# Optimization experiments

Measured on AMD Instinct MI355X. Metric: run time of the kernel, lower is better.

The kernel has to match this reference:

```python
import jax, jax.numpy as jnp
import numpy as np

C_IN, C_OUT, K, DG, PAD = 256, 256, 3, 2, 1
EPS = 1e-5


def setup_inputs() -> dict:
    key = jax.random.key(0)
    k = jax.random.split(key, 8)
    B, H, W = 4, 64, 64
    x = jax.random.normal(k[0], (B, C_IN, H, W), jnp.float32)
    # offset/mask conv (DCNv2 pack): 3 * dg * k * k output channels
    w_off = jax.random.normal(k[1], (3 * DG * K * K, C_IN, K, K), jnp.float32) * 0.01
    b_off = jnp.zeros((3 * DG * K * K,), jnp.float32)
    # main deformable conv weight
    w = jax.random.normal(k[2], (C_OUT, C_IN, K, K), jnp.float32) * (1.0 / np.sqrt(C_IN * K * K))
    b = jnp.zeros((C_OUT,), jnp.float32)
    # BatchNorm (eval mode: running stats)
    gamma = jnp.ones((C_OUT,), jnp.float32)
    beta = jnp.zeros((C_OUT,), jnp.float32)
    running_mean = jax.random.normal(k[3], (C_OUT,), jnp.float32) * 0.1
    running_var = jax.random.uniform(k[4], (C_OUT,), jnp.float32, 0.5, 1.5)
    return dict(x=x, w_off=w_off, b_off=b_off, w=w, b=b, gamma=gamma, beta=beta,
                running_mean=running_mean, running_var=running_var)


def _conv2d_same(x, w, b):
    y = jax.lax.conv_general_dilated(x, w, (1, 1), 'SAME',
                                     dimension_numbers=('NCHW', 'OIHW', 'NCHW'))
    return y + b[None, :, None, None]


def _deform_conv(x, w_off, b_off, w, b):
    B, C, H, W = x.shape
    K2 = K * K
    Cg = C // DG
    # offsets + modulation mask from internal conv (DCNv2 pack)
    om = _conv2d_same(x, w_off, b_off)            # [B, 3*DG*K2, H, W]
    o1, o2, m = jnp.split(om, 3, axis=1)
    mask = jax.nn.sigmoid(m).reshape(B, DG, 1, K2, H * W)
    off_y = o1.reshape(B, DG, K2, H, W)
    off_x = o2.reshape(B, DG, K2, H, W)
    # base sampling grid: output pixel + kernel tap - pad
    ki = jnp.arange(K)
    ky = (jnp.repeat(ki, K) - PAD).astype(jnp.float32)   # [K2]
    kx = (jnp.tile(ki, K) - PAD).astype(jnp.float32)     # [K2]
    py = off_y + ky[:, None, None] + jnp.arange(H, dtype=jnp.float32)[None, :, None]
    px = off_x + kx[:, None, None] + jnp.arange(W, dtype=jnp.float32)[None, None, :]
    y0 = jnp.floor(py)
    x0 = jnp.floor(px)
    ly = (py - y0).reshape(B, DG, 1, K2, H * W)
    lx = (px - x0).reshape(B, DG, 1, K2, H * W)
    y0i = y0.astype(jnp.int32)
    x0i = x0.astype(jnp.int32)
    xg = x.reshape(B, DG, Cg, H * W)

    def gather(yi, xi):
        # zero-padded bilinear corner gather, per deformable group
        valid = (yi >= 0) & (yi < H) & (xi >= 0) & (xi < W)
        lin = jnp.clip(yi, 0, H - 1) * W + jnp.clip(xi, 0, W - 1)
        v = jnp.take_along_axis(xg[:, :, :, None, :],
                                lin.reshape(B, DG, 1, K2, H * W), axis=-1)
        return v * valid.reshape(B, DG, 1, K2, H * W)

    val = (gather(y0i, x0i) * (1 - ly) * (1 - lx)
           + gather(y0i, x0i + 1) * (1 - ly) * lx
           + gather(y0i + 1, x0i) * ly * (1 - lx)
           + gather(y0i + 1, x0i + 1) * ly * lx)
    val = val * mask                               # [B, DG, Cg, K2, H*W]
    wr = w.reshape(C_OUT, DG, Cg, K2)
    out = jnp.einsum('bgckn,ogck->bon', val, wr).reshape(B, C_OUT, H, W)
    return out + b[None, :, None, None]


def reference(x, w_off, b_off, w, b, gamma, beta, running_mean, running_var):
    y = _deform_conv(x, w_off, b_off, w, b)
    inv = gamma / jnp.sqrt(running_var + EPS)
    y = (y - running_mean[None, :, None, None]) * inv[None, :, None, None] + beta[None, :, None, None]
    return jax.nn.relu(y)
```

## Files before the change

### kernel.cpp

```cpp
#include <hip/hip_runtime.h>
#include <math.h>

typedef __bf16 bf16x8 __attribute__((ext_vector_type(8)));
typedef float  f32x4  __attribute__((ext_vector_type(4)));
typedef int    i32x4  __attribute__((ext_vector_type(4)));

#define MFMA16(a, b, c) __builtin_amdgcn_mfma_f32_16x16x32_bf16((a), (b), (c), 0, 0, 0)

#define ATIDX(r, c) ((r) * 128 + (((c) ^ ((r) & 7)) * 8))

__global__ __launch_bounds__(256) void setup_kernel(
    const float* __restrict__ x, const float* __restrict__ w,
    const float* __restrict__ w_off, const float* __restrict__ bconv,
    const float* __restrict__ gamma, const float* __restrict__ beta,
    const float* __restrict__ mean, const float* __restrict__ var,
    __bf16* __restrict__ xT, __bf16* __restrict__ wFragD,
    __bf16* __restrict__ wFragO, float* __restrict__ sc,
    float* __restrict__ sh) {
  int t = threadIdx.x;
  if (blockIdx.x < 1024) {
    __shared__ float xs[64][65];
    int b = blockIdx.x >> 8, y = (blockIdx.x >> 2) & 63, cc = blockIdx.x & 3;
    const float* xb = x + (((size_t)b * 256 + cc * 64) * 64 + y) * 64;
    #pragma unroll
    for (int r = 0; r < 4; ++r) {
      int cl = r * 16 + (t >> 4), xc = (t & 15) * 4;
      f32x4 v = *(const f32x4*)(xb + (size_t)cl * 4096 + xc);
      xs[cl][xc] = v.x; xs[cl][xc + 1] = v.y;
      xs[cl][xc + 2] = v.z; xs[cl][xc + 3] = v.w;
    }
    __syncthreads();
    __bf16* dst = xT + (((size_t)b * 64 + y) * 64) * 256 + cc * 64;
    #pragma unroll
    for (int it = 0; it < 2; ++it) {
      int w2 = t + it * 256;
      int xc = w2 >> 3, cl8 = (w2 & 7) * 8;
      bf16x8 o;
      #pragma unroll
      for (int e = 0; e < 8; ++e) o[e] = (__bf16)xs[cl8 + e][xc];
      *(bf16x8*)(dst + (size_t)xc * 256 + cl8) = o;
    }
    return;
  }
  if (blockIdx.x < 1312) {
    int u = (blockIdx.x - 1024) * 256 + t;
    int lane = u & 63, ocb = (u >> 6) & 15, kc = (u >> 10) & 3, gk = u >> 12;
    int oc = ocb * 16 + (lane & 15);
    int cb = kc * 32 + (lane >> 4) * 8;
    int g = gk / 9, ktap = gk % 9;
    const float* src = w + ((size_t)oc * 256 + g * 128 + cb) * 9 + ktap;
    bf16x8 o;
    #pragma unroll
    for (int j = 0; j < 8; ++j) o[j] = (__bf16)src[(size_t)j * 9];
    *(bf16x8*)(wFragD + (size_t)u * 8) = o;
    return;
  }
  if (blockIdx.x < 1384) {
    int u = (blockIdx.x - 1312) * 256 + t;
    int lane = u & 63, ocq = (u >> 6) & 3, kc = (u >> 8) & 7, tap = u >> 11;
    int oc = ocq * 16 + (lane & 15);
    int cb = kc * 32 + (lane >> 4) * 8;
    bf16x8 o;
    #pragma unroll
    for (int j = 0; j < 8; ++j) o[j] = (__bf16)0.f;
    if (oc < 54) {
      const float* src = w_off + ((size_t)oc * 256 + cb) * 9 + tap;
      #pragma unroll
      for (int j = 0; j < 8; ++j) o[j] = (__bf16)src[(size_t)j * 9];
    }
    *(bf16x8*)(wFragO + (size_t)u * 8) = o;
    return;
  }
  if (t < 256) {
    float s = gamma[t] * rsqrtf(var[t] + 1e-5f);
    sc[t] = s;
    sh[t] = (bconv[t] - mean[t]) * s + beta[t];
  }
}

struct PhaseC {
  f32x4 swgtv[18 * 64];
  i32x4 slinv[18 * 64];
  __bf16 atile[2][2][64 * 128];
};
union FusedLDS {
  __bf16 rowbuf[3 * 66 * 256];
  PhaseC c;
};

__global__ __launch_bounds__(1024) void fused_kernel(
    const __bf16* __restrict__ xT, const __bf16* __restrict__ wFragD,
    const __bf16* __restrict__ wFragO, const float* __restrict__ b_off,
    const float* __restrict__ sc, const float* __restrict__ sh,
    float* __restrict__ out) {
  __shared__ __attribute__((aligned(16))) FusedLDS U;
  __shared__ float omrow[2][54 * 64];
  int t = threadIdx.x;
  int b = blockIdx.x >> 6, y = blockIdx.x & 63;
  int lane = t & 63, wv = t >> 6;
  int l15 = lane & 15, quad = lane >> 4;
  const __bf16* xTb = xT + (size_t)b * 64 * 64 * 256;
  bf16x8 z8;
  #pragma unroll
  for (int e = 0; e < 8; ++e) z8[e] = (__bf16)0.f;

  for (int i = t; i < 3 * 66 * 32; i += 1024) {
    int c = i & 31, px66 = (i >> 5) % 66, dy = i / 2112;
    int y2 = y + dy - 1, x2 = px66 - 1;
    bf16x8 v = z8;
    if (y2 >= 0 && y2 < 64 && x2 >= 0 && x2 < 64)
      v = *(const bf16x8*)(xTb + ((size_t)y2 * 64 + x2) * 256 + c * 8);
    *(bf16x8*)&U.rowbuf[dy * 16896 + px66 * 256 + ((c ^ (px66 & 7)) * 8)] = v;
  }
  __syncthreads();

  {
    int kh = wv & 1, pxt = (wv >> 1) & 3, ocd = wv >> 3;
    f32x4 acc0 = {0.f, 0.f, 0.f, 0.f};
    f32x4 acc1 = {0.f, 0.f, 0.f, 0.f};
    for (int tap = 0; tap < 9; ++tap) {
      int dy = tap / 3, dxs = tap % 3;
      const __bf16* bb =
          wFragO + ((size_t)(tap * 8 + kh * 4) * 4 + ocd * 2) * 512 + lane * 8;
      bf16x8 Bf0[4], Bf1[4];
      #pragma unroll
      for (int kcl = 0; kcl < 4; ++kcl) {
        Bf0[kcl] = *(const bf16x8*)(bb + (size_t)kcl * 4 * 512);
        Bf1[kcl] = *(const bf16x8*)(bb + (size_t)kcl * 4 * 512 + 512);
      }
      int p0 = pxt * 16 + l15 + dxs;
      const __bf16* rb = U.rowbuf + dy * 16896;
      #pragma unroll
      for (int kcl = 0; kcl < 4; ++kcl) {
        int c = (kh * 4 + kcl) * 4 + quad;
        bf16x8 a0 = *(const bf16x8*)&rb[p0 * 256 + ((c ^ (p0 & 7)) * 8)];
        acc0 = MFMA16(a0, Bf0[kcl], acc0);
        acc1 = MFMA16(a0, Bf1[kcl], acc1);
      }
    }
    #pragma unroll
    for (int fo = 0; fo < 2; ++fo) {
      f32x4 v = fo ? acc1 : acc0;
      int oc = (ocd * 2 + fo) * 16 + l15;
      if (oc < 54)
        *(f32x4*)&omrow[kh][oc * 64 + pxt * 16 + quad * 4] = v;
    }
  }
  __syncthreads();

  for (int i = t; i < 18 * 64; i += 1024) {
    int gk = i >> 6, pb = i & 63;
    int k = gk % 9;
    float oy = omrow[0][gk * 64 + pb] + omrow[1][gk * 64 + pb] + b_off[gk];
    float ox = omrow[0][(18 + gk) * 64 + pb] + omrow[1][(18 + gk) * 64 + pb]
             + b_off[18 + gk];
    float mz = omrow[0][(36 + gk) * 64 + pb] + omrow[1][(36 + gk) * 64 + pb]
             + b_off[36 + gk];
    float mv = 1.f / (1.f + expf(-mz));
    float py  = (float)(y + (k / 3) - 1) + oy;
    float pxf = (float)(pb + (k % 3) - 1) + ox;
    float y0f = floorf(py), x0f = floorf(pxf);
    int y0 = (int)y0f, x0 = (int)x0f;
    float ly = py - y0f, lx = pxf - x0f;
    int y1 = y0 + 1, x1 = x0 + 1;
    bool vy0 = (y0 >= 0) && (y0 < 64), vy1 = (y1 >= 0) && (y1 < 64);
    bool vx0 = (x0 >= 0) && (x0 < 64), vx1 = (x1 >= 0) && (x1 < 64);
    int cy0 = min(max(y0, 0), 63), cy1 = min(max(y1, 0), 63);
    int cx0 = min(max(x0, 0), 63), cx1 = min(max(x1, 0), 63);
    f32x4 sv;
    sv.x = (vy0 && vx0) ? (1.f - ly) * (1.f - lx) * mv : 0.f;
    sv.y = (vy0 && vx1) ? (1.f - ly) * lx * mv : 0.f;
    sv.z = (vy1 && vx0) ? ly * (1.f - lx) * mv : 0.f;
    sv.w = (vy1 && vx1) ? ly * lx * mv : 0.f;
    i32x4 lv;
    lv.x = (cy0 * 64 + cx0) * 256;
    lv.y = (cy0 * 64 + cx1) * 256;
    lv.z = (cy1 * 64 + cx0) * 256;
    lv.w = (cy1 * 64 + cx1) * 256;
    U.c.swgtv[i] = sv;
    U.c.slinv[i] = lv;
  }

  int ocp = wv & 7, fmh = wv >> 3;
  f32x4 acc[2][2];
  #pragma unroll
  for (int fm = 0; fm < 2; ++fm)
    #pragma unroll
    for (int fn = 0; fn < 2; ++fn)
      acc[fm][fn] = (f32x4){0.f, 0.f, 0.f, 0.f};

  __syncthreads();

  int ch0 = l15 * 8;
  int p = wv * 4 + quad;

  #pragma unroll
  for (int t2 = 0; t2 < 2; ++t2) {
    f32x4 sv = U.c.swgtv[t2 * 64 + p];
    i32x4 lv = U.c.slinv[t2 * 64 + p];
    const __bf16* xg = xTb + ch0;
    bf16x8 c0 = *(const bf16x8*)(xg + lv.x);
    bf16x8 c1 = *(const bf16x8*)(xg + lv.y);
    bf16x8 c2 = *(const bf16x8*)(xg + lv.z);
    bf16x8 c3 = *(const bf16x8*)(xg + lv.w);
    bf16x8 o;
    #pragma unroll
    for (int e = 0; e < 8; ++e)
      o[e] = (__bf16)(sv.x * (float)c0[e] + sv.y * (float)c1[e]
                    + sv.z * (float)c2[e] + sv.w * (float)c3[e]);
    *(bf16x8*)&U.c.atile[0][t2][ATIDX(p, l15)] = o;
  }

  for (int iv = 0; iv < 9; ++iv) {
    int buf = iv & 1;
    int t0 = 2 * iv;
    __syncthreads();
    bf16x8 Bf0[8];
    const __bf16* bb0 =
        wFragD + ((size_t)(t0 * 4) * 16 + ocp * 2) * 512 + lane * 8;
    #pragma unroll
    for (int kc = 0; kc < 4; ++kc) {
      Bf0[kc * 2]     = *(const bf16x8*)(bb0 + (size_t)kc * 16 * 512);
      Bf0[kc * 2 + 1] = *(const bf16x8*)(bb0 + (size_t)kc * 16 * 512 + 512);
    }
    bf16x8 cr[2][4];
    f32x4 sv[2];
    if (iv < 8) {
      #pragma unroll
      for (int t2 = 0; t2 < 2; ++t2) {
        int gn = t0 + 2 + t2;
        const __bf16* xg = xTb + (gn / 9) * 128 + ch0;
        sv[t2] = U.c.swgtv[gn * 64 + p];
        i32x4 lv = U.c.slinv[gn * 64 + p];
        cr[t2][0] = *(const bf16x8*)(xg + lv.x);
        cr[t2][1] = *(const bf16x8*)(xg + lv.y);
        cr[t2][2] = *(const bf16x8*)(xg + lv.z);
        cr[t2][3] = *(const bf16x8*)(xg + lv.w);
      }
    }
    __builtin_amdgcn_sched_barrier(0);
    {
      const __bf16* at0 = U.c.atile[buf][0];
      #pragma unroll
      for (int kc = 0; kc < 4; ++kc) {
        #pragma unroll
        for (int fm = 0; fm < 2; ++fm) {
          bf16x8 a = *(const bf16x8*)
              &at0[ATIDX((fmh * 2 + fm) * 16 + l15, kc * 4 + quad)];
          acc[fm][0] = MFMA16(a, Bf0[kc * 2],     acc[fm][0]);
          acc[fm][1] = MFMA16(a, Bf0[kc * 2 + 1], acc[fm][1]);
        }
      }
    }
    bf16x8 Bf1[8];
    const __bf16* bb1 = bb0 + (size_t)4 * 16 * 512;
    #pragma unroll
    for (int kc = 0; kc < 4; ++kc) {
      Bf1[kc * 2]     = *(const bf16x8*)(bb1 + (size_t)kc * 16 * 512);
      Bf1[kc * 2 + 1] = *(const bf16x8*)(bb1 + (size_t)kc * 16 * 512 + 512);
    }
    {
      const __bf16* at1 = U.c.atile[buf][1];
      #pragma unroll
      for (int kc = 0; kc < 4; ++kc) {
        #pragma unroll
        for (int fm = 0; fm < 2; ++fm) {
          bf16x8 a = *(const bf16x8*)
              &at1[ATIDX((fmh * 2 + fm) * 16 + l15, kc * 4 + quad)];
          acc[fm][0] = MFMA16(a, Bf1[kc * 2],     acc[fm][0]);
          acc[fm][1] = MFMA16(a, Bf1[kc * 2 + 1], acc[fm][1]);
        }
      }
    }
    __builtin_amdgcn_sched_barrier(0);
    if (iv < 8) {
      #pragma unroll
      for (int t2 = 0; t2 < 2; ++t2) {
        __bf16* dst = U.c.atile[buf ^ 1][t2];
        bf16x8 o;
        #pragma unroll
        for (int e = 0; e < 8; ++e)
          o[e] = (__bf16)(sv[t2].x * (float)cr[t2][0][e]
                        + sv[t2].y * (float)cr[t2][1][e]
                        + sv[t2].z * (float)cr[t2][2][e]
                        + sv[t2].w * (float)cr[t2][3][e]);
        *(bf16x8*)&dst[ATIDX(p, l15)] = o;
      }
    }
  }

  #pragma unroll
  for (int fm = 0; fm < 2; ++fm) {
    #pragma unroll
    for (int fn = 0; fn < 2; ++fn) {
      int oc = (ocp * 2 + fn) * 16 + l15;
      float s = sc[oc], h = sh[oc];
      f32x4 v = acc[fm][fn];
      f32x4 r = {fmaxf(v.x * s + h, 0.f), fmaxf(v.y * s + h, 0.f),
                 fmaxf(v.z * s + h, 0.f), fmaxf(v.w * s + h, 0.f)};
      int pxs = (fmh * 2 + fm) * 16 + quad * 4;
      *(f32x4*)(out + (((size_t)b * 256 + oc) * 64 + y) * 64 + pxs) = r;
    }
  }
}

extern "C" void kernel_launch(void* const* d_in, const int* in_sizes, int n_in,
                              void* d_out, int out_size, void* d_ws, size_t ws_size,
                              hipStream_t stream) {
  const float* x     = (const float*)d_in[0];
  const float* w_off = (const float*)d_in[1];
  const float* b_off = (const float*)d_in[2];
  const float* w     = (const float*)d_in[3];
  const float* bconv = (const float*)d_in[4];
  const float* gamma = (const float*)d_in[5];
  const float* beta  = (const float*)d_in[6];
  const float* rmean = (const float*)d_in[7];
  const float* rvar  = (const float*)d_in[8];
  float* out = (float*)d_out;

  __bf16* xT     = (__bf16*)d_ws;
  __bf16* wFragD = (__bf16*)((char*)d_ws + 8388608);
  __bf16* wFragO = (__bf16*)((char*)d_ws + 9568256);
  float*  sc     = (float*)((char*)d_ws + 9863168);
  float*  sh     = (float*)((char*)d_ws + 9864192);

  setup_kernel<<<1385, 256, 0, stream>>>(
      x, w, w_off, bconv, gamma, beta, rmean, rvar, xT, wFragD, wFragO, sc, sh);
  fused_kernel<<<4 * 64, 1024, 0, stream>>>(xT, wFragD, wFragO, b_off, sc, sh, out);
}
```

Baseline: 138.4 us.

## Warp-specialize deformable conv: 8 MFMA waves, 8 bilinear gather producer waves

Splits the 16 waves of each block into two roles. Waves 0-7 run all the MFMA work, each covering 32 output channels across all 64 pixels with a larger accumulator. Waves 8-15 do the bilinear gather and interpolation that fills the next double-buffered A tile. Before, every wave interleaved gather and MFMA. The goal is to overlap the latency-bound gathers with matrix math across separate waves, at the cost of more accumulator registers per compute wave and idle producer waves in the last iteration.

New measurement: 131.0 us. 5.3% less time.

```diff
diff --git a/kernel.cpp b/kernel.cpp
--- a/kernel.cpp
+++ b/kernel.cpp
@@ -181,125 +181,143 @@
     U.c.slinv[i] = lv;
   }
 
-  int ocp = wv & 7, fmh = wv >> 3;
-  f32x4 acc[2][2];
+  f32x4 acc[4][2];
   #pragma unroll
-  for (int fm = 0; fm < 2; ++fm)
+  for (int fm = 0; fm < 4; ++fm)
     #pragma unroll
     for (int fn = 0; fn < 2; ++fn)
       acc[fm][fn] = (f32x4){0.f, 0.f, 0.f, 0.f};
 
   __syncthreads();
 
-  int ch0 = l15 * 8;
-  int p = wv * 4 + quad;
-
-  #pragma unroll
-  for (int t2 = 0; t2 < 2; ++t2) {
-    f32x4 sv = U.c.swgtv[t2 * 64 + p];
-    i32x4 lv = U.c.slinv[t2 * 64 + p];
-    const __bf16* xg = xTb + ch0;
-    bf16x8 c0 = *(const bf16x8*)(xg + lv.x);
-    bf16x8 c1 = *(const bf16x8*)(xg + lv.y);
-    bf16x8 c2 = *(const bf16x8*)(xg + lv.z);
-    bf16x8 c3 = *(const bf16x8*)(xg + lv.w);
-    bf16x8 o;
-    #pragma unroll
-    for (int e = 0; e < 8; ++e)
-      o[e] = (__bf16)(sv.x * (float)c0[e] + sv.y * (float)c1[e]
-                    + sv.z * (float)c2[e] + sv.w * (float)c3[e]);
-    *(bf16x8*)&U.c.atile[0][t2][ATIDX(p, l15)] = o;
+  if (wv >= 8) {
+    int pt = (wv - 8) * 64 + lane;
+    #pragma unroll
+    for (int t2 = 0; t2 < 2; ++t2) {
+      #pragma unroll
+      for (int s = 0; s < 2; ++s) {
+        int idx = s * 512 + pt;
+        int px = idx >> 4, ck = idx & 15;
+        f32x4 sv = U.c.swgtv[t2 * 64 + px];
+        i32x4 lv = U.c.slinv[t2 * 64 + px];
+        const __bf16* xg = xTb + ck * 8;
+        bf16x8 c0 = *(const bf16x8*)(xg + lv.x);
+        bf16x8 c1 = *(const bf16x8*)(xg + lv.y);
+        bf16x8 c2 = *(const bf16x8*)(xg + lv.z);
+        bf16x8 c3 = *(const bf16x8*)(xg + lv.w);
+        bf16x8 o;
+        #pragma unroll
+        for (int e = 0; e < 8; ++e)
+          o[e] = (__bf16)(sv.x * (float)c0[e] + sv.y * (float)c1[e]
+                        + sv.z * (float)c2[e] + sv.w * (float)c3[e]);
+        *(bf16x8*)&U.c.atile[0][t2][ATIDX(px, ck)] = o;
+      }
+    }
   }
 
   for (int iv = 0; iv < 9; ++iv) {
-    int buf = iv & 1;
-    int t0 = 2 * iv;
     __syncthreads();
-    bf16x8 Bf0[8];
-    const __bf16* bb0 =
-        wFragD + ((size_t)(t0 * 4) * 16 + ocp * 2) * 512 + lane * 8;
-    #pragma unroll
-    for (int kc = 0; kc < 4; ++kc) {
-      Bf0[kc * 2]     = *(const bf16x8*)(bb0 + (size_t)kc * 16 * 512);
-      Bf0[kc * 2 + 1] = *(const bf16x8*)(bb0 + (size_t)kc * 16 * 512 + 512);
-    }
-    bf16x8 cr[2][4];
-    f32x4 sv[2];
-    if (iv < 8) {
+    if (wv < 8) {
+      bf16x8 Bf0[8];
+      #pragma unroll
+      for (int kc = 0; kc < 4; ++kc) {
+        const __bf16* bp =
+            wFragD + ((size_t)((2 * iv) * 4 + kc) * 16 + wv * 2) * 512
+            + lane * 8;
+        Bf0[kc * 2]     = *(const bf16x8*)bp;
+        Bf0[kc * 2 + 1] = *(const bf16x8*)(bp + 512);
+      }
+      __builtin_amdgcn_sched_barrier(0);
+      {
+        const __bf16* at0 = U.c.atile[iv & 1][0];
+        #pragma unroll
+        for (int kc = 0; kc < 4; ++kc) {
+          #pragma unroll
+          for (int fm = 0; fm < 4; ++fm) {
+            bf16x8 a = *(const bf16x8*)
+                &at0[ATIDX(fm * 16 + l15, kc * 4 + quad)];
+            acc[fm][0] = MFMA16(a, Bf0[kc * 2],     acc[fm][0]);
+            acc[fm][1] = MFMA16(a, Bf0[kc * 2 + 1], acc[fm][1]);
+          }
+        }
+      }
+      bf16x8 Bf1[8];
+      #pragma unroll
+      for (int kc = 0; kc < 4; ++kc) {
+        const __bf16* bp =
+            wFragD + ((size_t)((2 * iv + 1) * 4 + kc) * 16 + wv * 2) * 512
+            + lane * 8;
+        Bf1[kc * 2]     = *(const bf16x8*)bp;
+        Bf1[kc * 2 + 1] = *(const bf16x8*)(bp + 512);
+      }
+      {
+        const __bf16* at1 = U.c.atile[iv & 1][1];
+        #pragma unroll
+        for (int kc = 0; kc < 4; ++kc) {
+          #pragma unroll
+          for (int fm = 0; fm < 4; ++fm) {
+            bf16x8 a = *(const bf16x8*)
+                &at1[ATIDX(fm * 16 + l15, kc * 4 + quad)];
+            acc[fm][0] = MFMA16(a, Bf1[kc * 2],     acc[fm][0]);
+            acc[fm][1] = MFMA16(a, Bf1[kc * 2 + 1], acc[fm][1]);
+          }
+        }
+      }
+    } else if (iv < 8) {
+      int pt = (wv - 8) * 64 + lane;
+      bf16x8 cr[2][2][4];
+      f32x4 sv[2][2];
+      int dsta[2][2];
       #pragma unroll
       for (int t2 = 0; t2 < 2; ++t2) {
-        int gn = t0 + 2 + t2;
-        const __bf16* xg = xTb + (gn / 9) * 128 + ch0;
-        sv[t2] = U.c.swgtv[gn * 64 + p];
-        i32x4 lv = U.c.slinv[gn * 64 + p];
-        cr[t2][0] = *(const bf16x8*)(xg + lv.x);
-        cr[t2][1] = *(const bf16x8*)(xg + lv.y);
-        cr[t2][2] = *(const bf16x8*)(xg + lv.z);
-        cr[t2][3] = *(const bf16x8*)(xg + lv.w);
-      }
-    }
-    __builtin_amdgcn_sched_barrier(0);
-    {
-      const __bf16* at0 = U.c.atile[buf][0];
-      #pragma unroll
-      for (int kc = 0; kc < 4; ++kc) {
-        #pragma unroll
-        for (int fm = 0; fm < 2; ++fm) {
-          bf16x8 a = *(const bf16x8*)
-              &at0[ATIDX((fmh * 2 + fm) * 16 + l15, kc * 4 + quad)];
-          acc[fm][0] = MFMA16(a, Bf0[kc * 2],     acc[fm][0]);
-          acc[fm][1] = MFMA16(a, Bf0[kc * 2 + 1], acc[fm][1]);
+        int gn = 2 * iv + 2 + t2;
+        const __bf16* xg = xTb + (gn / 9) * 128;
+        #pragma unroll
+        for (int s = 0; s < 2; ++s) {
+          int idx = s * 512 + pt;
+          int px = idx >> 4, ck = idx & 15;
+          sv[t2][s] = U.c.swgtv[gn * 64 + px];
+          i32x4 lv = U.c.slinv[gn * 64 + px];
+          const __bf16* xc = xg + ck * 8;
+          cr[t2][s][0] = *(const bf16x8*)(xc + lv.x);
+          cr[t2][s][1] = *(const bf16x8*)(xc + lv.y);
+          cr[t2][s][2] = *(const bf16x8*)(xc + lv.z);
+          cr[t2][s][3] = *(const bf16x8*)(xc + lv.w);
+          dsta[t2][s] = ATIDX(px, ck);
         }
       }
-    }
-    bf16x8 Bf1[8];
-    const __bf16* bb1 = bb0 + (size_t)4 * 16 * 512;
-    #pragma unroll
-    for (int kc = 0; kc < 4; ++kc) {
-      Bf1[kc * 2]     = *(const bf16x8*)(bb1 + (size_t)kc * 16 * 512);
-      Bf1[kc * 2 + 1] = *(const bf16x8*)(bb1 + (size_t)kc * 16 * 512 + 512);
-    }
-    {
-      const __bf16* at1 = U.c.atile[buf][1];
-      #pragma unroll
-      for (int kc = 0; kc < 4; ++kc) {
-        #pragma unroll
-        for (int fm = 0; fm < 2; ++fm) {
-          bf16x8 a = *(const bf16x8*)
-              &at1[ATIDX((fmh * 2 + fm) * 16 + l15, kc * 4 + quad)];
-          acc[fm][0] = MFMA16(a, Bf1[kc * 2],     acc[fm][0]);
-          acc[fm][1] = MFMA16(a, Bf1[kc * 2 + 1], acc[fm][1]);
+      __builtin_amdgcn_sched_barrier(0);
+      #pragma unroll
+      for (int t2 = 0; t2 < 2; ++t2) {
+        __bf16* dst = U.c.atile[(iv + 1) & 1][t2];
+        #pragma unroll
+        for (int s = 0; s < 2; ++s) {
+          bf16x8 o;
+          #pragma unroll
+          for (int e = 0; e < 8; ++e)
+            o[e] = (__bf16)(sv[t2][s].x * (float)cr[t2][s][0][e]
+                          + sv[t2][s].y * (float)cr[t2][s][1][e]
+                          + sv[t2][s].z * (float)cr[t2][s][2][e]
+                          + sv[t2][s].w * (float)cr[t2][s][3][e]);
+          *(bf16x8*)&dst[dsta[t2][s]] = o;
         }
       }
     }
-    __builtin_amdgcn_sched_barrier(0);
-    if (iv < 8) {
-      #pragma unroll
-      for (int t2 = 0; t2 < 2; ++t2) {
-        __bf16* dst = U.c.atile[buf ^ 1][t2];
-        bf16x8 o;
-        #pragma unroll
-        for (int e = 0; e < 8; ++e)
-          o[e] = (__bf16)(sv[t2].x * (float)cr[t2][0][e]
-                        + sv[t2].y * (float)cr[t2][1][e]
-                        + sv[t2].z * (float)cr[t2][2][e]
-                        + sv[t2].w * (float)cr[t2][3][e]);
-        *(bf16x8*)&dst[ATIDX(p, l15)] = o;
-      }
-    }
-  }
-
-  #pragma unroll
-  for (int fm = 0; fm < 2; ++fm) {
+  }
+
+  if (wv < 8) {
     #pragma unroll
     for (int fn = 0; fn < 2; ++fn) {
-      int oc = (ocp * 2 + fn) * 16 + l15;
+      int oc = wv * 32 + fn * 16 + l15;
       float s = sc[oc], h = sh[oc];
-      f32x4 v = acc[fm][fn];
-      f32x4 r = {fmaxf(v.x * s + h, 0.f), fmaxf(v.y * s + h, 0.f),
-                 fmaxf(v.z * s + h, 0.f), fmaxf(v.w * s + h, 0.f)};
-      int pxs = (fmh * 2 + fm) * 16 + quad * 4;
-      *(f32x4*)(out + (((size_t)b * 256 + oc) * 64 + y) * 64 + pxs) = r;
+      #pragma unroll
+      for (int fm = 0; fm < 4; ++fm) {
+        f32x4 v = acc[fm][fn];
+        f32x4 r = {fmaxf(v.x * s + h, 0.f), fmaxf(v.y * s + h, 0.f),
+                   fmaxf(v.z * s + h, 0.f), fmaxf(v.w * s + h, 0.f)};
+        int pxs = fm * 16 + quad * 4;
+        *(f32x4*)(out + (((size_t)b * 256 + oc) * 64 + y) * 64 + pxs) = r;
+      }
     }
   }
 }
```
